# Performance work log

Hardware: AMD Instinct MI355X
Metric: run time of the kernel (lower is better)

## Reference

```python
import jax, jax.numpy as jnp
import numpy as np

D_MODEL = 1024
N_HEAD = 16
D_HEAD = D_MODEL // N_HEAD
D_FF = 4096
EPS = 1e-5


def _layernorm(x, gamma, beta):
    mu = jnp.mean(x, axis=-1, keepdims=True)
    var = jnp.mean(jnp.square(x - mu), axis=-1, keepdims=True)
    return (x - mu) * jax.lax.rsqrt(var + EPS) * gamma + beta


def setup_inputs() -> dict:
    key = jax.random.key(0)
    ks = jax.random.split(key, 16)
    s = 1.0 / np.sqrt(D_MODEL)
    sf = 1.0 / np.sqrt(D_FF)
    return {
        "src": jax.random.normal(ks[0], (8, 1024, D_MODEL), dtype=jnp.float32),
        "Wq": jax.random.uniform(ks[1], (D_MODEL, D_MODEL), jnp.float32, -s, s),
        "bq": jnp.zeros((D_MODEL,), jnp.float32),
        "Wk": jax.random.uniform(ks[2], (D_MODEL, D_MODEL), jnp.float32, -s, s),
        "bk": jnp.zeros((D_MODEL,), jnp.float32),
        "Wv": jax.random.uniform(ks[3], (D_MODEL, D_MODEL), jnp.float32, -s, s),
        "bv": jnp.zeros((D_MODEL,), jnp.float32),
        "Wo": jax.random.uniform(ks[4], (D_MODEL, D_MODEL), jnp.float32, -s, s),
        "bo": jnp.zeros((D_MODEL,), jnp.float32),
        "W1": jax.random.uniform(ks[5], (D_MODEL, D_FF), jnp.float32, -s, s),
        "b1": jnp.zeros((D_FF,), jnp.float32),
        "W2": jax.random.uniform(ks[6], (D_FF, D_MODEL), jnp.float32, -sf, sf),
        "b2": jnp.zeros((D_MODEL,), jnp.float32),
        "g1": jnp.ones((D_MODEL,), jnp.float32),
        "beta1": jnp.zeros((D_MODEL,), jnp.float32),
        "g2": jnp.ones((D_MODEL,), jnp.float32),
        "beta2": jnp.zeros((D_MODEL,), jnp.float32),
    }


def reference(src, Wq, bq, Wk, bk, Wv, bv, Wo, bo, W1, b1, W2, b2, g1, beta1, g2, beta2):
    B, S, _ = src.shape
    x = _layernorm(src, g1, beta1)
    # QKV projections -> [B, H, S, Dh]
    def split_heads(t):
        return t.reshape(B, S, N_HEAD, D_HEAD).transpose(0, 2, 1, 3)
    q = split_heads(x @ Wq + bq)
    k = split_heads(x @ Wk + bk)
    v = split_heads(x @ Wv + bv)
    # SymbolicAttention (canonical graph): softmax(q k^T / sqrt(d_head)) v
    scores = jnp.einsum('bhqd,bhkd->bhqk', q, k) / np.sqrt(D_HEAD).astype(np.float32)
    attn = jax.nn.softmax(scores, axis=-1)
    ctx = jnp.einsum('bhqk,bhkd->bhqd', attn, v)
    ctx = ctx.transpose(0, 2, 1, 3).reshape(B, S, D_MODEL)
    src = src + (ctx @ Wo + bo)  # dropout is identity in eval
    y = _layernorm(src, g2, beta2)
    ffn = jax.nn.relu(y @ W1 + b1) @ W2 + b2
    return src + ffn
```

## Files before the change

kernel.cpp:

```cpp
#include <hip/hip_runtime.h>
#include <stdint.h>

#define D_MODEL 1024
#define N_HEAD  16
#define D_HEAD  64
#define D_FF    4096
#define SEQ     1024
#define BATCH   8
#define M_TOK   (BATCH*SEQ)

typedef __attribute__((ext_vector_type(8))) short bf16x8;
typedef __attribute__((ext_vector_type(4))) float f32x4;

__device__ __forceinline__ float bf2f(unsigned short u) {
    union { unsigned int u; float f; } x; x.u = ((unsigned int)u) << 16; return x.f;
}
__device__ __forceinline__ unsigned short f2bf(float f) {
    union { float f; unsigned int u; } x; x.f = f;
    unsigned int r = x.u + 0x7fffu + ((x.u >> 16) & 1u);
    return (unsigned short)(r >> 16);
}

typedef const __attribute__((address_space(1))) unsigned int* gas_t;
typedef __attribute__((address_space(3))) unsigned int* las_t;
__device__ __forceinline__ void gl_lds16(const unsigned short* g, unsigned short* l) {
    __builtin_amdgcn_global_load_lds((gas_t)g, (las_t)l, 16, 0, 0);
}

__global__ __launch_bounds__(256) void transpose_cvt(
        const float* __restrict__ src, unsigned short* __restrict__ dst,
        int R, int C)
{
    __shared__ float t[32][33];
    const int tx = threadIdx.x & 31, ty = threadIdx.x >> 5;
    const int c0 = blockIdx.x * 32, r0 = blockIdx.y * 32;
    #pragma unroll
    for (int i = 0; i < 32; i += 8)
        t[ty + i][tx] = src[(size_t)(r0 + ty + i) * C + c0 + tx];
    __syncthreads();
    #pragma unroll
    for (int i = 0; i < 32; i += 8)
        dst[(size_t)(c0 + ty + i) * R + r0 + tx] = f2bf(t[tx][ty + i]);
}

__global__ __launch_bounds__(256) void ln_kernel(
        const float* __restrict__ x, const float* __restrict__ g,
        const float* __restrict__ be, unsigned short* __restrict__ out)
{
    const int row = blockIdx.x, tid = threadIdx.x;
    const f32x4 v = *(const f32x4*)(x + (size_t)row * D_MODEL + tid * 4);
    float s  = v[0] + v[1] + v[2] + v[3];
    float ss = v[0]*v[0] + v[1]*v[1] + v[2]*v[2] + v[3]*v[3];
    #pragma unroll
    for (int o = 1; o < 64; o <<= 1) { s += __shfl_xor(s, o); ss += __shfl_xor(ss, o); }
    __shared__ float sa[4], sb[4];
    const int wv = tid >> 6;
    if ((tid & 63) == 0) { sa[wv] = s; sb[wv] = ss; }
    __syncthreads();
    s  = sa[0] + sa[1] + sa[2] + sa[3];
    ss = sb[0] + sb[1] + sb[2] + sb[3];
    const float mu   = s * (1.0f / D_MODEL);
    const float rstd = rsqrtf(ss * (1.0f / D_MODEL) - mu * mu + 1e-5f);
    const f32x4 gv = *(const f32x4*)(g  + tid * 4);
    const f32x4 bv = *(const f32x4*)(be + tid * 4);
    unsigned short w[4];
    #pragma unroll
    for (int j = 0; j < 4; j++) w[j] = f2bf((v[j] - mu) * rstd * gv[j] + bv[j]);
    *(uint2*)(out + (size_t)row * D_MODEL + tid * 4) = *(uint2*)w;
}

template<int MODE>
__global__ __launch_bounds__(256) void gemm_bf16_tn(
        const unsigned short* __restrict__ A,
        const unsigned short* __restrict__ BT,
        const float* __restrict__ bias,
        const float* __restrict__ bias2,
        const float* __restrict__ bias3,
        const float* __restrict__ resid,
        void* __restrict__ Cout,
        int M, int N, int K)
{
    constexpr bool SWAP = (MODE != 3);
    __shared__ unsigned short As[128 * 64];
    __shared__ unsigned short Bs[128 * 64];

    const int tid  = threadIdx.x;
    const int wave = tid >> 6, lane = tid & 63;
    const int quad = lane >> 4, l16 = lane & 15;

    int m0, n0;
    if (MODE == 2) {
        const int G = gridDim.x;
        const int f = blockIdx.x + G * blockIdx.y;
        m0 = ((f & 7) + 8 * ((f >> 3) / G)) * 128;
        n0 = ((f >> 3) % G) * 128;
    } else {
        m0 = blockIdx.y * 128;
        n0 = blockIdx.x * 128;
    }
    const int wm = (wave >> 1) * 64, wn = (wave & 1) * 64;

    const int st_row = wave * 8 + ((tid >> 3) & 7);
    const int st_g   = (tid & 7) ^ ((tid >> 3) & 7);
    const unsigned short* gA = A  + (size_t)(m0 + st_row) * K + st_g * 8;
    const unsigned short* gB = BT + (size_t)(n0 + st_row) * K + st_g * 8;
    unsigned short* lA = As + wave * 512;
    unsigned short* lB = Bs + wave * 512;
    const int rx = l16 & 7;

    f32x4 acc[4][4] = {};

    for (int k0 = 0; k0 < K; k0 += 64) {
        __syncthreads();
        #pragma unroll
        for (int j = 0; j < 4; j++) {
            gl_lds16(gA + (size_t)j * 32 * K + k0, lA + j * 2048);
            gl_lds16(gB + (size_t)j * 32 * K + k0, lB + j * 2048);
        }
        __syncthreads();

        #pragma unroll
        for (int h = 0; h < 2; h++) {
            bf16x8 af[4], bfr[4];
            #pragma unroll
            for (int mi = 0; mi < 4; mi++)
                af[mi] = *(const bf16x8*)(As + (wm + mi * 16 + l16) * 64
                                          + ((h * 4 + quad) ^ rx) * 8);
            #pragma unroll
            for (int ni = 0; ni < 4; ni++)
                bfr[ni] = *(const bf16x8*)(Bs + (wn + ni * 16 + l16) * 64
                                           + ((h * 4 + quad) ^ rx) * 8);
            #pragma unroll
            for (int mi = 0; mi < 4; mi++)
                #pragma unroll
                for (int ni = 0; ni < 4; ni++)
                    acc[mi][ni] = SWAP
                        ? __builtin_amdgcn_mfma_f32_16x16x32_bf16(
                              bfr[ni], af[mi], acc[mi][ni], 0, 0, 0)
                        : __builtin_amdgcn_mfma_f32_16x16x32_bf16(
                              af[mi], bfr[ni], acc[mi][ni], 0, 0, 0);
        }
    }

    if (SWAP) {
        #pragma unroll
        for (int mi = 0; mi < 4; mi++) {
            const int row = m0 + wm + mi * 16 + l16;
            #pragma unroll
            for (int ni = 0; ni < 4; ni++) {
                const int col = n0 + wn + ni * 16 + quad * 4;
                const f32x4 bs4 = *(const f32x4*)(bias + col);
                if (MODE == 1) {
                    unsigned short w[4];
                    #pragma unroll
                    for (int r = 0; r < 4; r++)
                        w[r] = f2bf(fmaxf(acc[mi][ni][r] + bs4[r], 0.0f));
                    *(uint2*)((unsigned short*)Cout + (size_t)row * N + col)
                        = *(uint2*)w;
                } else {
                    const f32x4 rv = *(const f32x4*)(resid + (size_t)row * N + col);
                    f32x4 o;
                    #pragma unroll
                    for (int r = 0; r < 4; r++)
                        o[r] = acc[mi][ni][r] + bs4[r] + rv[r];
                    *(f32x4*)((float*)Cout + (size_t)row * N + col) = o;
                }
            }
        }
    } else {
        #pragma unroll
        for (int mi = 0; mi < 4; mi++) {
            const int row_b = m0 + wm + mi * 16 + quad * 4;
            #pragma unroll
            for (int ni = 0; ni < 4; ni++) {
                const int col = n0 + wn + ni * 16 + l16;
                if (col < 2048) {
                    const float sc  = (col < 1024) ? 0.125f : 1.0f;
                    const float bsv = (col < 1024) ? bias[col] : bias2[col - 1024];
                    unsigned short* dst = (unsigned short*)Cout
                        + (size_t)(col >> 10) * M_TOK * 1024;
                    #pragma unroll
                    for (int r = 0; r < 4; r++)
                        dst[(size_t)(row_b + r) * 1024 + (col & 1023)] =
                            f2bf((acc[mi][ni][r] + bsv) * sc);
                } else {
                    const int cc = col - 2048;
                    const float bsv = bias3[cc];
                    const int bb = row_b >> 10, s = row_b & 1023;
                    const int h = cc >> 6, dd = cc & 63;
                    unsigned short w[4];
                    #pragma unroll
                    for (int r = 0; r < 4; r++)
                        w[r] = f2bf(acc[mi][ni][r] + bsv);
                    *(uint2*)((unsigned short*)Cout + (size_t)2 * M_TOK * 1024
                              + ((size_t)((bb * 16 + h) * 64 + dd)) * 1024 + s)
                        = *(uint2*)w;
                }
            }
        }
    }
}

#define ASTR 72
__global__ __launch_bounds__(256) void attn_mfma(
        const unsigned short* __restrict__ Q,
        const unsigned short* __restrict__ K,
        const unsigned short* __restrict__ VT,
        unsigned short* __restrict__ CTX)
{
    __shared__ unsigned short Ks[64 * ASTR];
    __shared__ unsigned short Vs[64 * ASTR];
    __shared__ unsigned short Ps[128 * ASTR];

    const int tid  = threadIdx.x;
    const int wave = tid >> 6, lane = tid & 63;
    const int quad = lane >> 4, l16 = lane & 15;
    const int bh = blockIdx.y;
    const int q0 = blockIdx.x * 128;
    const size_t baseQ = (size_t)(bh >> 4) * SEQ * D_MODEL + (size_t)(bh & 15) * D_HEAD;
    const size_t baseV = (size_t)bh * D_HEAD * SEQ;
    const int strip = wave * 32;

    bf16x8 qf[2][2];
    #pragma unroll
    for (int mt = 0; mt < 2; mt++)
        #pragma unroll
        for (int h = 0; h < 2; h++)
            qf[mt][h] = *(const bf16x8*)(Q + baseQ
                        + (size_t)(q0 + strip + mt * 16 + l16) * D_MODEL
                        + h * 32 + quad * 8);

    f32x4 of[2][4] = {};
    float l_p[2][4] = {};

    for (int c = 0; c < SEQ / 64; c++) {
        const int k0 = c * 64;
        __syncthreads();
        #pragma unroll
        for (int u = tid; u < 512; u += 256) {
            const int r = u >> 3, g = (u & 7) * 8;
            *(uint4*)(Ks + r * ASTR + g) =
                *(const uint4*)(K + baseQ + (size_t)(k0 + r) * D_MODEL + g);
            *(uint4*)(Vs + r * ASTR + g) =
                *(const uint4*)(VT + baseV + (size_t)r * SEQ + k0 + g);
        }
        __syncthreads();

        bf16x8 kf[4][2];
        #pragma unroll
        for (int kt = 0; kt < 4; kt++)
            #pragma unroll
            for (int h = 0; h < 2; h++)
                kf[kt][h] = *(const bf16x8*)(Ks + (kt * 16 + l16) * ASTR + h * 32 + quad * 8);

        #pragma unroll
        for (int mt = 0; mt < 2; mt++) {
            f32x4 s[4] = {};
            #pragma unroll
            for (int h = 0; h < 2; h++)
                #pragma unroll
                for (int kt = 0; kt < 4; kt++)
                    s[kt] = __builtin_amdgcn_mfma_f32_16x16x32_bf16(
                            qf[mt][h], kf[kt][h], s[kt], 0, 0, 0);
            #pragma unroll
            for (int kt = 0; kt < 4; kt++)
                #pragma unroll
                for (int r = 0; r < 4; r++) {
                    const float p = __expf(s[kt][r]);
                    l_p[mt][r] += p;
                    Ps[(strip + mt * 16 + quad * 4 + r) * ASTR + kt * 16 + l16] = f2bf(p);
                }
        }

        bf16x8 pf[2][2];
        #pragma unroll
        for (int mt = 0; mt < 2; mt++)
            #pragma unroll
            for (int h = 0; h < 2; h++)
                pf[mt][h] = *(const bf16x8*)(Ps + (strip + mt * 16 + l16) * ASTR
                                             + h * 32 + quad * 8);
        #pragma unroll
        for (int nt = 0; nt < 4; nt++) {
            bf16x8 vf[2];
            #pragma unroll
            for (int h = 0; h < 2; h++)
                vf[h] = *(const bf16x8*)(Vs + (nt * 16 + l16) * ASTR + h * 32 + quad * 8);
            #pragma unroll
            for (int mt = 0; mt < 2; mt++)
                #pragma unroll
                for (int h = 0; h < 2; h++)
                    of[mt][nt] = __builtin_amdgcn_mfma_f32_16x16x32_bf16(
                            pf[mt][h], vf[h], of[mt][nt], 0, 0, 0);
        }
    }

    #pragma unroll
    for (int mt = 0; mt < 2; mt++) {
        float inv[4];
        #pragma unroll
        for (int r = 0; r < 4; r++) {
            float l = l_p[mt][r];
            #pragma unroll
            for (int o = 1; o < 16; o <<= 1) l += __shfl_xor(l, o);
            inv[r] = 1.0f / l;
        }
        #pragma unroll
        for (int nt = 0; nt < 4; nt++)
            #pragma unroll
            for (int r = 0; r < 4; r++)
                CTX[baseQ + (size_t)(q0 + strip + mt * 16 + quad * 4 + r) * D_MODEL
                    + nt * 16 + l16] = f2bf(of[mt][nt][r] * inv[r]);
    }
}

extern "C" void kernel_launch(void* const* d_in, const int* in_sizes, int n_in,
                              void* d_out, int out_size, void* d_ws, size_t ws_size,
                              hipStream_t stream)
{
    (void)in_sizes; (void)n_in; (void)out_size; (void)ws_size;
    const float* src = (const float*)d_in[0];
    const float* Wq  = (const float*)d_in[1];
    const float* bq  = (const float*)d_in[2];
    const float* Wk  = (const float*)d_in[3];
    const float* bk  = (const float*)d_in[4];
    const float* Wv  = (const float*)d_in[5];
    const float* bv  = (const float*)d_in[6];
    const float* Wo  = (const float*)d_in[7];
    const float* bo  = (const float*)d_in[8];
    const float* W1  = (const float*)d_in[9];
    const float* b1  = (const float*)d_in[10];
    const float* W2  = (const float*)d_in[11];
    const float* b2  = (const float*)d_in[12];
    const float* g1  = (const float*)d_in[13];
    const float* be1 = (const float*)d_in[14];
    const float* g2  = (const float*)d_in[15];
    const float* be2 = (const float*)d_in[16];
    float* out = (float*)d_out;

    unsigned short* wqkvT = (unsigned short*)d_ws;
    unsigned short* woT = wqkvT + (size_t)3 * 1024 * 1024;
    unsigned short* w1T = woT + 1024 * 1024;
    unsigned short* w2T = w1T + (size_t)4096 * 1024;
    unsigned short* xn  = w2T + (size_t)1024 * 4096;
    unsigned short* q   = xn  + (size_t)M_TOK * D_MODEL;
    unsigned short* k   = q   + (size_t)M_TOK * D_MODEL;
    unsigned short* vT  = k   + (size_t)M_TOK * D_MODEL;
    unsigned short* ctx = vT  + (size_t)M_TOK * D_MODEL;
    unsigned short* hid = ctx + (size_t)M_TOK * D_MODEL;

    const dim3 blk(256);

    transpose_cvt<<<dim3(32, 32),  blk, 0, stream>>>(Wq, wqkvT,                 1024, 1024);
    transpose_cvt<<<dim3(32, 32),  blk, 0, stream>>>(Wk, wqkvT + 1024 * 1024,   1024, 1024);
    transpose_cvt<<<dim3(32, 32),  blk, 0, stream>>>(Wv, wqkvT + 2 * 1024 * 1024, 1024, 1024);
    transpose_cvt<<<dim3(32, 32),  blk, 0, stream>>>(Wo, woT, 1024, 1024);
    transpose_cvt<<<dim3(128, 32), blk, 0, stream>>>(W1, w1T, 1024, 4096);
    transpose_cvt<<<dim3(32, 128), blk, 0, stream>>>(W2, w2T, 4096, 1024);

    ln_kernel<<<M_TOK, blk, 0, stream>>>(src, g1, be1, xn);

    gemm_bf16_tn<3><<<dim3(24, 64), blk, 0, stream>>>(
        xn, wqkvT, bq, bk, bv, nullptr, q, M_TOK, 3072, D_MODEL);

    attn_mfma<<<dim3(SEQ / 128, BATCH * N_HEAD), blk, 0, stream>>>(q, k, vT, ctx);

    gemm_bf16_tn<2><<<dim3(8, 64), blk, 0, stream>>>(
        ctx, woT, bo, nullptr, nullptr, src, out, M_TOK, D_MODEL, D_MODEL);

    ln_kernel<<<M_TOK, blk, 0, stream>>>(out, g2, be2, xn);

    gemm_bf16_tn<1><<<dim3(32, 64), blk, 0, stream>>>(
        xn, w1T, b1, nullptr, nullptr, nullptr, hid, M_TOK, D_FF, D_MODEL);

    gemm_bf16_tn<2><<<dim3(8, 64), blk, 0, stream>>>(
        hid, w2T, b2, nullptr, nullptr, out, out, M_TOK, D_MODEL, D_FF);
}
```

Baseline: 543.6 us.

## Add 256x256-tile ping-pong GEMM for QKV and FFN1 projections

Adds a 512-thread GEMM kernel with 256x256 output tiles, double-buffered direct global-to-LDS staging, interleaved quarter-tile MFMA phases with barriers and setprio, and swizzled LDS reads. The QKV and W1 GEMMs now use it, which raises data reuse per loaded tile and overlaps loads with MFMA work. The old GEMM is reduced to the residual epilogue path only. The trade-offs are heavy register and LDS use (128KB LDS per block), fewer blocks in flight, and a V-transpose epilogue that now writes scalar stores.

Result: faster. 504.1 us (-7.3%).

```diff
diff --git a/kernel.cpp b/kernel.cpp
--- a/kernel.cpp
+++ b/kernel.cpp
@@ -70,6 +70,221 @@
 }
 
 template<int MODE>
+__global__ __launch_bounds__(512, 2) void gemm256(
+        const unsigned short* __restrict__ A,
+        const unsigned short* __restrict__ BT,
+        const float* __restrict__ b1_,
+        const float* __restrict__ b2_,
+        const float* __restrict__ b3_,
+        void* __restrict__ Cout,
+        int M, int N, int K)
+{
+    (void)M;
+    __shared__ unsigned short As[32768];
+    __shared__ unsigned short Bs[32768];
+
+    const int tid  = threadIdx.x;
+    const int wave = tid >> 6, lane = tid & 63;
+    const int quad = lane >> 4, l16 = lane & 15;
+    const int wm = wave >> 2, wn = wave & 3;
+
+    const int m0 = blockIdx.y * 256;
+    const int n0 = blockIdx.x * 256;
+    const int NT = K >> 6;
+
+    const int st_row = tid >> 3;
+    const int st_g   = (tid & 7) ^ (st_row & 7);
+    const unsigned short* gA = A  + (size_t)(m0 + st_row) * K + st_g * 8;
+    const unsigned short* gB = BT + (size_t)(n0 + st_row) * K + st_g * 8;
+    unsigned short* lA = As + wave * 512;
+    unsigned short* lB = Bs + wave * 512;
+
+    const int aOff = (wm * 64 + l16) * 64;
+    const int bOff = (wn * 32 + l16) * 64;
+    const int s0s  = (quad ^ (l16 & 7)) * 8;
+    const int s1s  = s0s ^ 32;
+
+    f32x4 acc[8][4] = {};
+
+#define STAGE_A(T, H, D) \
+    do { gl_lds16(gA + (size_t)((H)*128   )*K + (size_t)(T)*64, lA + (D)*16384 + (H)*8192); \
+         gl_lds16(gA + (size_t)((H)*128+64)*K + (size_t)(T)*64, lA + (D)*16384 + (H)*8192 + 4096); } while(0)
+#define STAGE_B(T, H, D) \
+    do { gl_lds16(gB + (size_t)((H)*128   )*K + (size_t)(T)*64, lB + (D)*16384 + (H)*8192); \
+         gl_lds16(gB + (size_t)((H)*128+64)*K + (size_t)(T)*64, lB + (D)*16384 + (H)*8192 + 4096); } while(0)
+
+    STAGE_A(0, 0, 0); STAGE_B(0, 0, 0); STAGE_B(0, 1, 0); STAGE_A(0, 1, 0);
+    STAGE_A(1, 0, 1); STAGE_B(1, 0, 1); STAGE_B(1, 1, 1);
+    asm volatile("s_waitcnt vmcnt(6)" ::: "memory");
+    __builtin_amdgcn_s_barrier();
+    asm volatile("" ::: "memory");
+
+    for (int t = 0; t < NT; ++t) {
+        const int db = t & 1;
+        const unsigned short* Adb = As + db * 16384;
+        const unsigned short* Bdb = Bs + db * 16384;
+        bf16x8 af[4][2], bfA[2][2], bfB[2][2];
+
+        #pragma unroll
+        for (int mi = 0; mi < 4; ++mi) {
+            af[mi][0] = *(const bf16x8*)(Adb + aOff + mi * 1024 + s0s);
+            af[mi][1] = *(const bf16x8*)(Adb + aOff + mi * 1024 + s1s);
+        }
+        #pragma unroll
+        for (int ni = 0; ni < 2; ++ni) {
+            bfA[ni][0] = *(const bf16x8*)(Bdb + bOff + ni * 1024 + s0s);
+            bfA[ni][1] = *(const bf16x8*)(Bdb + bOff + ni * 1024 + s1s);
+        }
+        if (t + 1 < NT) STAGE_A(t + 1, 1, db ^ 1);
+        asm volatile("" ::: "memory");
+        __builtin_amdgcn_s_barrier();
+        asm volatile("s_waitcnt lgkmcnt(0)");
+        __builtin_amdgcn_s_setprio(1);
+        #pragma unroll
+        for (int mi = 0; mi < 4; ++mi)
+            #pragma unroll
+            for (int ni = 0; ni < 2; ++ni) {
+                acc[mi][ni] = __builtin_amdgcn_mfma_f32_16x16x32_bf16(
+                        bfA[ni][0], af[mi][0], acc[mi][ni], 0, 0, 0);
+                acc[mi][ni] = __builtin_amdgcn_mfma_f32_16x16x32_bf16(
+                        bfA[ni][1], af[mi][1], acc[mi][ni], 0, 0, 0);
+            }
+        __builtin_amdgcn_s_setprio(0);
+        asm volatile("" ::: "memory");
+        __builtin_amdgcn_s_barrier();
+        asm volatile("" ::: "memory");
+
+        #pragma unroll
+        for (int ni = 0; ni < 2; ++ni) {
+            bfB[ni][0] = *(const bf16x8*)(Bdb + 8192 + bOff + ni * 1024 + s0s);
+            bfB[ni][1] = *(const bf16x8*)(Bdb + 8192 + bOff + ni * 1024 + s1s);
+        }
+        if (t + 2 < NT) STAGE_A(t + 2, 0, db);
+        asm volatile("" ::: "memory");
+        __builtin_amdgcn_s_barrier();
+        asm volatile("s_waitcnt lgkmcnt(0)");
+        __builtin_amdgcn_s_setprio(1);
+        #pragma unroll
+        for (int mi = 0; mi < 4; ++mi)
+            #pragma unroll
+            for (int ni = 0; ni < 2; ++ni) {
+                acc[mi][2 + ni] = __builtin_amdgcn_mfma_f32_16x16x32_bf16(
+                        bfB[ni][0], af[mi][0], acc[mi][2 + ni], 0, 0, 0);
+                acc[mi][2 + ni] = __builtin_amdgcn_mfma_f32_16x16x32_bf16(
+                        bfB[ni][1], af[mi][1], acc[mi][2 + ni], 0, 0, 0);
+            }
+        __builtin_amdgcn_s_setprio(0);
+        asm volatile("" ::: "memory");
+        __builtin_amdgcn_s_barrier();
+        asm volatile("" ::: "memory");
+
+        #pragma unroll
+        for (int mi = 0; mi < 4; ++mi) {
+            af[mi][0] = *(const bf16x8*)(Adb + 8192 + aOff + mi * 1024 + s0s);
+            af[mi][1] = *(const bf16x8*)(Adb + 8192 + aOff + mi * 1024 + s1s);
+        }
+        if (t + 2 < NT) STAGE_B(t + 2, 0, db);
+        asm volatile("" ::: "memory");
+        __builtin_amdgcn_s_barrier();
+        asm volatile("s_waitcnt lgkmcnt(0)");
+        __builtin_amdgcn_s_setprio(1);
+        #pragma unroll
+        for (int mi = 0; mi < 4; ++mi)
+            #pragma unroll
+            for (int ni = 0; ni < 2; ++ni) {
+                acc[4 + mi][ni] = __builtin_amdgcn_mfma_f32_16x16x32_bf16(
+                        bfA[ni][0], af[mi][0], acc[4 + mi][ni], 0, 0, 0);
+                acc[4 + mi][ni] = __builtin_amdgcn_mfma_f32_16x16x32_bf16(
+                        bfA[ni][1], af[mi][1], acc[4 + mi][ni], 0, 0, 0);
+            }
+        __builtin_amdgcn_s_setprio(0);
+        asm volatile("" ::: "memory");
+        __builtin_amdgcn_s_barrier();
+        asm volatile("" ::: "memory");
+
+        if (t + 2 < NT) {
+            STAGE_B(t + 2, 1, db);
+            asm volatile("s_waitcnt vmcnt(6)" ::: "memory");
+        } else {
+            asm volatile("s_waitcnt vmcnt(0)" ::: "memory");
+        }
+        __builtin_amdgcn_s_barrier();
+        __builtin_amdgcn_s_setprio(1);
+        #pragma unroll
+        for (int mi = 0; mi < 4; ++mi)
+            #pragma unroll
+            for (int ni = 0; ni < 2; ++ni) {
+                acc[4 + mi][2 + ni] = __builtin_amdgcn_mfma_f32_16x16x32_bf16(
+                        bfB[ni][0], af[mi][0], acc[4 + mi][2 + ni], 0, 0, 0);
+                acc[4 + mi][2 + ni] = __builtin_amdgcn_mfma_f32_16x16x32_bf16(
+                        bfB[ni][1], af[mi][1], acc[4 + mi][2 + ni], 0, 0, 0);
+            }
+        __builtin_amdgcn_s_setprio(0);
+        asm volatile("" ::: "memory");
+        __builtin_amdgcn_s_barrier();
+        asm volatile("" ::: "memory");
+    }
+#undef STAGE_A
+#undef STAGE_B
+
+    if (MODE == 1) {
+        unsigned short* dst = (unsigned short*)Cout;
+        #pragma unroll
+        for (int f = 0; f < 8; ++f) {
+            const int row = m0 + (f >> 2) * 128 + wm * 64 + (f & 3) * 16 + l16;
+            #pragma unroll
+            for (int g = 0; g < 4; ++g) {
+                const int col = n0 + (g >> 1) * 128 + wn * 32 + (g & 1) * 16 + quad * 4;
+                const f32x4 bs4 = *(const f32x4*)(b1_ + col);
+                unsigned short w[4];
+                #pragma unroll
+                for (int r = 0; r < 4; ++r)
+                    w[r] = f2bf(fmaxf(acc[f][g][r] + bs4[r], 0.0f));
+                *(uint2*)(dst + (size_t)row * N + col) = *(uint2*)w;
+            }
+        }
+    } else {
+        const int rt = n0 >> 10;
+        if (rt < 2) {
+            unsigned short* dst = (unsigned short*)Cout + (size_t)rt * M_TOK * 1024;
+            const float sc = (rt == 0) ? 0.125f : 1.0f;
+            const float* bs = (rt == 0) ? b1_ : b2_;
+            const int nb = n0 & 1023;
+            #pragma unroll
+            for (int f = 0; f < 8; ++f) {
+                const int row = m0 + (f >> 2) * 128 + wm * 64 + (f & 3) * 16 + l16;
+                #pragma unroll
+                for (int g = 0; g < 4; ++g) {
+                    const int col = nb + (g >> 1) * 128 + wn * 32 + (g & 1) * 16 + quad * 4;
+                    const f32x4 bs4 = *(const f32x4*)(bs + col);
+                    unsigned short w[4];
+                    #pragma unroll
+                    for (int r = 0; r < 4; ++r)
+                        w[r] = f2bf((acc[f][g][r] + bs4[r]) * sc);
+                    *(uint2*)(dst + (size_t)row * 1024 + col) = *(uint2*)w;
+                }
+            }
+        } else {
+            unsigned short* vdst = (unsigned short*)Cout + (size_t)2 * M_TOK * 1024;
+            const int nb = n0 - 2048;
+            #pragma unroll
+            for (int f = 0; f < 8; ++f) {
+                const int row = m0 + (f >> 2) * 128 + wm * 64 + (f & 3) * 16 + l16;
+                const int bb = row >> 10, s = row & 1023;
+                #pragma unroll
+                for (int g = 0; g < 4; ++g) {
+                    const int cc = nb + (g >> 1) * 128 + wn * 32 + (g & 1) * 16 + quad * 4;
+                    #pragma unroll
+                    for (int r = 0; r < 4; ++r)
+                        vdst[((size_t)(bb * 1024 + cc + r)) * 1024 + s]
+                            = f2bf(acc[f][g][r] + b3_[cc + r]);
+                }
+            }
+        }
+    }
+}
+
+template<int MODE>
 __global__ __launch_bounds__(256) void gemm_bf16_tn(
         const unsigned short* __restrict__ A,
         const unsigned short* __restrict__ BT,
@@ -80,7 +295,7 @@
         void* __restrict__ Cout,
         int M, int N, int K)
 {
-    constexpr bool SWAP = (MODE != 3);
+    (void)bias2; (void)bias3;
     __shared__ unsigned short As[128 * 64];
     __shared__ unsigned short Bs[128 * 64];
 
@@ -134,69 +349,24 @@
             for (int mi = 0; mi < 4; mi++)
                 #pragma unroll
                 for (int ni = 0; ni < 4; ni++)
-                    acc[mi][ni] = SWAP
-                        ? __builtin_amdgcn_mfma_f32_16x16x32_bf16(
-                              bfr[ni], af[mi], acc[mi][ni], 0, 0, 0)
-                        : __builtin_amdgcn_mfma_f32_16x16x32_bf16(
-                              af[mi], bfr[ni], acc[mi][ni], 0, 0, 0);
-        }
-    }
-
-    if (SWAP) {
-        #pragma unroll
-        for (int mi = 0; mi < 4; mi++) {
-            const int row = m0 + wm + mi * 16 + l16;
-            #pragma unroll
-            for (int ni = 0; ni < 4; ni++) {
-                const int col = n0 + wn + ni * 16 + quad * 4;
-                const f32x4 bs4 = *(const f32x4*)(bias + col);
-                if (MODE == 1) {
-                    unsigned short w[4];
-                    #pragma unroll
-                    for (int r = 0; r < 4; r++)
-                        w[r] = f2bf(fmaxf(acc[mi][ni][r] + bs4[r], 0.0f));
-                    *(uint2*)((unsigned short*)Cout + (size_t)row * N + col)
-                        = *(uint2*)w;
-                } else {
-                    const f32x4 rv = *(const f32x4*)(resid + (size_t)row * N + col);
-                    f32x4 o;
-                    #pragma unroll
-                    for (int r = 0; r < 4; r++)
-                        o[r] = acc[mi][ni][r] + bs4[r] + rv[r];
-                    *(f32x4*)((float*)Cout + (size_t)row * N + col) = o;
-                }
-            }
-        }
-    } else {
-        #pragma unroll
-        for (int mi = 0; mi < 4; mi++) {
-            const int row_b = m0 + wm + mi * 16 + quad * 4;
-            #pragma unroll
-            for (int ni = 0; ni < 4; ni++) {
-                const int col = n0 + wn + ni * 16 + l16;
-                if (col < 2048) {
-                    const float sc  = (col < 1024) ? 0.125f : 1.0f;
-                    const float bsv = (col < 1024) ? bias[col] : bias2[col - 1024];
-                    unsigned short* dst = (unsigned short*)Cout
-                        + (size_t)(col >> 10) * M_TOK * 1024;
-                    #pragma unroll
-                    for (int r = 0; r < 4; r++)
-                        dst[(size_t)(row_b + r) * 1024 + (col & 1023)] =
-                            f2bf((acc[mi][ni][r] + bsv) * sc);
-                } else {
-                    const int cc = col - 2048;
-                    const float bsv = bias3[cc];
-                    const int bb = row_b >> 10, s = row_b & 1023;
-                    const int h = cc >> 6, dd = cc & 63;
-                    unsigned short w[4];
-                    #pragma unroll
-                    for (int r = 0; r < 4; r++)
-                        w[r] = f2bf(acc[mi][ni][r] + bsv);
-                    *(uint2*)((unsigned short*)Cout + (size_t)2 * M_TOK * 1024
-                              + ((size_t)((bb * 16 + h) * 64 + dd)) * 1024 + s)
-                        = *(uint2*)w;
-                }
-            }
+                    acc[mi][ni] = __builtin_amdgcn_mfma_f32_16x16x32_bf16(
+                              bfr[ni], af[mi], acc[mi][ni], 0, 0, 0);
+        }
+    }
+
+    #pragma unroll
+    for (int mi = 0; mi < 4; mi++) {
+        const int row = m0 + wm + mi * 16 + l16;
+        #pragma unroll
+        for (int ni = 0; ni < 4; ni++) {
+            const int col = n0 + wn + ni * 16 + quad * 4;
+            const f32x4 bs4 = *(const f32x4*)(bias + col);
+            const f32x4 rv = *(const f32x4*)(resid + (size_t)row * N + col);
+            f32x4 o;
+            #pragma unroll
+            for (int r = 0; r < 4; r++)
+                o[r] = acc[mi][ni][r] + bs4[r] + rv[r];
+            *(f32x4*)((float*)Cout + (size_t)row * N + col) = o;
         }
     }
 }
@@ -349,6 +519,7 @@
     unsigned short* hid = ctx + (size_t)M_TOK * D_MODEL;
 
     const dim3 blk(256);
+    const dim3 blk512(512);
 
     transpose_cvt<<<dim3(32, 32),  blk, 0, stream>>>(Wq, wqkvT,                 1024, 1024);
     transpose_cvt<<<dim3(32, 32),  blk, 0, stream>>>(Wk, wqkvT + 1024 * 1024,   1024, 1024);
@@ -359,8 +530,8 @@
 
     ln_kernel<<<M_TOK, blk, 0, stream>>>(src, g1, be1, xn);
 
-    gemm_bf16_tn<3><<<dim3(24, 64), blk, 0, stream>>>(
-        xn, wqkvT, bq, bk, bv, nullptr, q, M_TOK, 3072, D_MODEL);
+    gemm256<3><<<dim3(12, 32), blk512, 0, stream>>>(
+        xn, wqkvT, bq, bk, bv, q, M_TOK, 3072, D_MODEL);
 
     attn_mfma<<<dim3(SEQ / 128, BATCH * N_HEAD), blk, 0, stream>>>(q, k, vT, ctx);
 
@@ -369,8 +540,8 @@
 
     ln_kernel<<<M_TOK, blk, 0, stream>>>(out, g2, be2, xn);
 
-    gemm_bf16_tn<1><<<dim3(32, 64), blk, 0, stream>>>(
-        xn, w1T, b1, nullptr, nullptr, nullptr, hid, M_TOK, D_FF, D_MODEL);
+    gemm256<1><<<dim3(16, 32), blk512, 0, stream>>>(
+        xn, w1T, b1, nullptr, nullptr, hid, M_TOK, D_FF, D_MODEL);
 
     gemm_bf16_tn<2><<<dim3(8, 64), blk, 0, stream>>>(
         hid, w2T, b2, nullptr, nullptr, out, out, M_TOK, D_MODEL, D_FF);
```
